# Kernel tuning notes

Hardware: AMD Instinct MI355X
Metric: run time of the kernel (lower is better)

Reference implementation:

```python
import jax, jax.numpy as jnp
import numpy as np

# ---- config (matches init_kwargs) ----
B, CIN, IMG = 4, 3, 129
PATCH, STRIDE, PAD = 4, 1, 1
DIM = CIN * PATCH * PATCH          # 48, Token_performer input dim
EMB = 256                          # out_channel -> in_dim -> emb
M = EMB // 2                       # kernel_ratio=0.5 random features
UP = 2                             # up_scale
EPS = 1e-8


def layernorm(x, g, b):
    mu = x.mean(-1, keepdims=True)
    var = ((x - mu) ** 2).mean(-1, keepdims=True)
    return (x - mu) / jnp.sqrt(var + 1e-5) * g + b


def unfold(x, k=PATCH, pad=PAD):
    # torch nn.Unfold, stride=1: output [B, C*k*k, L*L], channel order (c, kh, kw)
    Bs, C, H, W = x.shape
    xp = jnp.pad(x, ((0, 0), (0, 0), (pad, pad), (pad, pad)))
    L = H + 2 * pad - k + 1
    cols = jnp.stack([xp[:, :, i:i + L, j:j + L]
                      for i in range(k) for j in range(k)], axis=2)  # [B,C,k*k,L,L]
    return cols.reshape(Bs, C * k * k, L * L)


def prm_exp(x, w):
    # Performer positive random features: exp(w@x - |x|^2/2)/sqrt(m)
    xd = 0.5 * jnp.sum(x * x, axis=-1, keepdims=True)          # [B,T,1]
    wtx = jnp.einsum('btd,md->btm', x, w)                       # [B,T,M]
    return jnp.exp(wtx - xd) / jnp.sqrt(jnp.float32(w.shape[0]))


def upsample_bilinear_ac(x, scale):
    # nn.UpsamplingBilinear2d => align_corners=True
    Bs, C, H, W = x.shape
    Ho, Wo = H * scale, W * scale
    def coords(n_in, n_out):
        f = jnp.arange(n_out, dtype=jnp.float32) * (n_in - 1) / (n_out - 1)
        i0 = jnp.clip(jnp.floor(f).astype(jnp.int32), 0, n_in - 2)
        return i0, f - i0.astype(jnp.float32)
    h0, th = coords(H, Ho)
    w0, tw = coords(W, Wo)
    xh = x[:, :, h0, :] * (1 - th)[None, None, :, None] + x[:, :, h0 + 1, :] * th[None, None, :, None]
    return xh[:, :, :, w0] * (1 - tw) + xh[:, :, :, w0 + 1] * tw


def setup_inputs() -> dict:
    key = jax.random.key(0)
    ks = jax.random.split(key, 8)
    def n(k, shape, s=0.02):
        return jax.random.normal(k, shape, dtype=jnp.float32) * s
    return dict(
        x=jax.random.normal(ks[0], (B, CIN, IMG, IMG), dtype=jnp.float32),
        g1=jnp.ones((DIM,), jnp.float32), b1=jnp.zeros((DIM,), jnp.float32),
        w_kqv=n(ks[1], (DIM, 3 * EMB)), b_kqv=jnp.zeros((3 * EMB,), jnp.float32),
        w_prm=jax.random.normal(ks[2], (M, EMB), dtype=jnp.float32) * 0.7,  # ~ orthogonal*sqrt(m)
        w_proj=n(ks[3], (EMB, EMB)), b_proj=jnp.zeros((EMB,), jnp.float32),
        g2=jnp.ones((EMB,), jnp.float32), b2=jnp.zeros((EMB,), jnp.float32),
        w_mlp1=n(ks[4], (EMB, EMB)), b_mlp1=jnp.zeros((EMB,), jnp.float32),
        w_mlp2=n(ks[5], (EMB, EMB)), b_mlp2=jnp.zeros((EMB,), jnp.float32),
    )


def reference(x, g1, b1, w_kqv, b_kqv, w_prm, w_proj, b_proj, g2, b2,
              w_mlp1, b_mlp1, w_mlp2, b_mlp2):
    Bs = x.shape[0]
    t = unfold(x).transpose(0, 2, 1)                     # [B, T, DIM], T = 128*128
    h = layernorm(t, g1, b1)
    kqv = h @ w_kqv + b_kqv                              # [B, T, 3*EMB]
    k, q, v = jnp.split(kqv, 3, axis=-1)                 # torch split order: k, q, v
    kp, qp = prm_exp(k, w_prm), prm_exp(q, w_prm)        # [B, T, M]
    D = jnp.einsum('btm,bm->bt', qp, kp.sum(axis=1))[..., None]   # [B,T,1]
    kptv = jnp.einsum('btn,btm->bnm', v, kp)             # [B, EMB, M]
    y = jnp.einsum('btm,bnm->btn', qp, kptv) / (D + EPS) # [B, T, EMB]
    y = v + (y @ w_proj + b_proj)                        # skip uses v
    z = layernorm(y, g2, b2)
    y = y + (jax.nn.gelu(z @ w_mlp1 + b_mlp1, approximate=False) @ w_mlp2 + b_mlp2)
    T = y.shape[1]
    S = int(np.sqrt(T))
    img = y.transpose(0, 2, 1).reshape(Bs, EMB, S, S)    # [B, 256, 128, 128]
    return upsample_bilinear_ac(img, UP)                 # [B, 256, 256, 256]
```

## Files before the change

kernel.cpp:

```cpp
#include <hip/hip_runtime.h>
#include <math.h>

#define TOK   16384
#define DIM   48
#define EMB   256
#define MF    128
#define IMGsz 129

typedef __attribute__((ext_vector_type(8))) short    bf16x8;
typedef __attribute__((ext_vector_type(8))) unsigned short u16x8;
typedef __attribute__((ext_vector_type(4))) float    f32x4;

__device__ __forceinline__ ushort f2bf(float f) {
    union { float f; unsigned u; } v; v.f = f;
    unsigned u = v.u;
    return (ushort)((u + 0x7fffu + ((u >> 16) & 1u)) >> 16);
}
__device__ __forceinline__ float bf2f(ushort h) {
    union { unsigned u; float f; } v; v.u = ((unsigned)h) << 16; return v.f;
}

#define SWZ64(r,c)  ((r)*64  + (((((c)>>3) ^ ((r)&7)) & 7) << 3) + ((c)&7))
#define SWZ256(r,c) ((r)*256 + (((((c)>>3) ^ ((r)&7))) << 3) + ((c)&7))

__device__ __forceinline__ int fragmajor(int n, int k, int KC) {
    return (((n >> 4)*KC + (k >> 5))*4 + ((k >> 3) & 3))*128 + (n & 15)*8 + (k & 7);
}

__global__ __launch_bounds__(256) void kprep(
    const float* __restrict__ w_kqv, const float* __restrict__ b_kqv,
    const float* __restrict__ w_prm,
    const float* __restrict__ w_mlp1, const float* __restrict__ w_mlp2,
    ushort* __restrict__ Wbig, ushort* __restrict__ wT2, float* __restrict__ bkq)
{
    __shared__ float redp[64][4];
    int blk = blockIdx.x, tid = threadIdx.x;
    if (blk < 256) {
        if (tid < 64) {
            float v = (tid < DIM) ? w_kqv[tid*768 + 512 + blk] : 0.f;
            Wbig[fragmajor(blk, tid, 2)] = f2bf(v);
        }
    } else if (blk < 512) {
        int isQ = (blk >= 384);
        int m = blk - (isQ ? 384 : 256);
        int d = tid & 63, part = tid >> 6;
        float s = 0.f;
        if (d < 48) {
            const float* wr = w_kqv + d*768 + (isQ ? 256 : 0);
            const float* pr = w_prm + m*256;
            for (int n = part*64; n < part*64 + 64; n++) s += wr[n]*pr[n];
        }
        redp[d][part] = s;
        __syncthreads();
        if (tid < 64)
            Wbig[fragmajor((isQ ? 384 : 256) + m, tid, 2)] =
                f2bf(redp[tid][0]+redp[tid][1]+redp[tid][2]+redp[tid][3]);
    } else if (blk < 640) {
        int isQ = (blk >= 576);
        int j = blk - (isQ ? 576 : 512);
        int i = tid & 63, part = tid >> 6;
        int off = isQ ? 256 : 0;
        float s = 0.f;
        for (int n = part*64; n < part*64 + 64; n++) {
            float wi = (i < 48) ? w_kqv[i*768 + off + n] : (i == 48 ? b_kqv[off + n] : 0.f);
            float wj = (j < 48) ? w_kqv[j*768 + off + n] : (j == 48 ? b_kqv[off + n] : 0.f);
            s += wi*wj;
        }
        redp[i][part] = s;
        __syncthreads();
        if (tid < 64)
            Wbig[fragmajor((isQ ? 576 : 512) + j, tid, 2)] =
                f2bf(redp[tid][0]+redp[tid][1]+redp[tid][2]+redp[tid][3]);
    } else if (blk < 1152) {
        int w = (blk >= 896);
        int n = blk - (w ? 896 : 640);
        const float* src = w ? w_mlp2 : w_mlp1;
        wT2[w*65536 + fragmajor(n, tid, 8)] = f2bf(src[tid*256 + n]);
    } else {
        float s = 0.f;
        int m = tid & 127, off = (tid >= 128) ? 256 : 0;
        for (int n = 0; n < 256; n++) s += w_prm[m*256 + n]*b_kqv[off + n];
        bkq[tid] = s;
    }
}

__global__ __launch_bounds__(256, 3) void k1_mfma(
    const float* __restrict__ x, const float* __restrict__ g1, const float* __restrict__ b1,
    const ushort* __restrict__ Wbig, const float* __restrict__ b_kqv,
    const float* __restrict__ bkq,
    ushort* __restrict__ vfrag_out, ushort* __restrict__ vT_out,
    ushort* __restrict__ kpT_out, ushort* __restrict__ qp_out)
{
    __shared__ __align__(16) ushort h_bf[32*64];
    __shared__ __align__(16) ushort vt_bf[32*256];
    __shared__ float xdp[4][32][2];
    __shared__ float xd2[32][2];
    __shared__ float red1[32][8], red2[32][8];
    __shared__ float mu_s[32], iv_s[32];
    float* t_s = (float*)vt_bf;

    const int blk = blockIdx.x;
    const int b  = blk >> 9;
    const int t0 = (blk & 511) << 5;
    const int tid = threadIdx.x;
    const int wid = tid >> 6;
    const int l15 = tid & 15, l4 = (tid >> 4) & 3;

    for (int e = tid; e < 32*DIM; e += 256) {
        int tok = e / DIM, j = e - tok*DIM;
        int t = t0 + tok;
        int lh = t >> 7, lw = t & 127;
        int c = j >> 4, kh = (j >> 2) & 3, kw = j & 3;
        int ih = lh + kh - 1, iw = lw + kw - 1;
        float val = 0.f;
        if (ih >= 0 && ih < IMGsz && iw >= 0 && iw < IMGsz)
            val = x[((b*3 + c)*IMGsz + ih)*IMGsz + iw];
        t_s[tok*DIM + j] = val;
    }
    __syncthreads();

    {
        int tg = tid >> 3, sl = tid & 7;
        const float* tr = &t_s[tg*DIM + sl*6];
        float s1 = 0.f, s2 = 0.f;
        #pragma unroll
        for (int j = 0; j < 6; j++) { float a = tr[j]; s1 += a; s2 = fmaf(a, a, s2); }
        red1[tg][sl] = s1; red2[tg][sl] = s2;
        __syncthreads();
        if (tid < 32) {
            float a = 0.f, q = 0.f;
            #pragma unroll
            for (int j = 0; j < 8; j++) { a += red1[tid][j]; q += red2[tid][j]; }
            float mu = a * (1.f/DIM);
            mu_s[tid] = mu;
            iv_s[tid] = rsqrtf(q*(1.f/DIM) - mu*mu + 1e-5f);
        }
        __syncthreads();
        float mu = mu_s[tg], iv = iv_s[tg];
        float hv[6];
        #pragma unroll
        for (int j = 0; j < 6; j++) hv[j] = (tr[j]-mu)*iv;
        #pragma unroll
        for (int j = 0; j < 6; j++) {
            int c = sl*6 + j;
            h_bf[SWZ64(tg, c)] = f2bf(hv[j]*g1[c] + b1[c]);
        }
        int c0 = 48 + sl*2;
        h_bf[SWZ64(tg, c0    )] = (sl == 0) ? (ushort)0x3F80 : (ushort)0;
        h_bf[SWZ64(tg, c0 + 1)] = 0;
    }
    __syncthreads();

    f32x4 acc[10][2];
    #pragma unroll
    for (int j = 0; j < 10; j++)
        #pragma unroll
        for (int m = 0; m < 2; m++) { acc[j][m][0]=0.f; acc[j][m][1]=0.f; acc[j][m][2]=0.f; acc[j][m][3]=0.f; }
    #pragma unroll
    for (int kc = 0; kc < 2; kc++) {
        int ch = ((kc*4 + l4) ^ (l15 & 7)) << 3;
        bf16x8 a0 = *(const bf16x8*)&h_bf[ l15      *64 + ch];
        bf16x8 a1 = *(const bf16x8*)&h_bf[(16 + l15)*64 + ch];
        #pragma unroll
        for (int j = 0; j < 10; j++) {
            int tile = wid + 4*j;
            bf16x8 bb = *(const bf16x8*)&Wbig[(((tile*2 + kc)*4 + l4)*16 + l15)*8];
            acc[j][0] = __builtin_amdgcn_mfma_f32_16x16x32_bf16(a0, bb, acc[j][0], 0, 0, 0);
            acc[j][1] = __builtin_amdgcn_mfma_f32_16x16x32_bf16(a1, bb, acc[j][1], 0, 0, 0);
        }
    }

    #pragma unroll
    for (int j = 0; j < 4; j++) {
        int col = (wid + 4*j)*16 + l15;
        float bias = b_kqv[512 + col];
        #pragma unroll
        for (int m = 0; m < 2; m++)
            #pragma unroll
            for (int r = 0; r < 4; r++) {
                int row = m*16 + l4*4 + r;
                vt_bf[row*256 + col] = f2bf(acc[j][m][r] + bias);
            }
    }
    #pragma unroll
    for (int m = 0; m < 2; m++)
        #pragma unroll
        for (int r = 0; r < 4; r++) {
            int row = m*16 + l4*4 + r;
            float hv = bf2f(h_bf[SWZ64(row, wid*16 + l15)]);
            float sk = acc[8][m][r]*hv, sq = acc[9][m][r]*hv;
            #pragma unroll
            for (int msk = 8; msk >= 1; msk >>= 1) {
                sk += __shfl_xor(sk, msk);
                sq += __shfl_xor(sq, msk);
            }
            if (l15 == 0) { xdp[wid][row][0] = sk; xdp[wid][row][1] = sq; }
        }
    __syncthreads();
    if (tid < 64) {
        int row = tid >> 1, ty = tid & 1;
        xd2[row][ty] = 0.5f*(xdp[0][row][ty] + xdp[1][row][ty] + xdp[2][row][ty] + xdp[3][row][ty]);
    }

    {
        ushort* dst = vT_out + ((size_t)(b*EMB + tid))*TOK + t0;
        #pragma unroll
        for (int t8 = 0; t8 < 4; t8++) {
            u16x8 pk8;
            #pragma unroll
            for (int j = 0; j < 8; j++) pk8[j] = vt_bf[(t8*8 + j)*256 + tid];
            *(u16x8*)&dst[t8*8] = pk8;
        }
    }
    {
        u16x8 pk8[4];
        #pragma unroll
        for (int m = 0; m < 2; m++)
            #pragma unroll
            for (int nt = 0; nt < 4; nt++)
                #pragma unroll
                for (int r = 0; r < 4; r++) {
                    int row = m*16 + l4*4 + r;
                    int col = wid*64 + nt*16 + l15;
                    int idx = m*16 + nt*4 + r;
                    pk8[idx >> 3][idx & 7] = vt_bf[row*256 + col];
                }
        ushort* dst = vfrag_out + (size_t)blk*8192 + tid*32;
        #pragma unroll
        for (int i = 0; i < 4; i++) *(u16x8*)&dst[i*8] = pk8[i];
    }
    __syncthreads();

    const float scale = 0.08838834764831845f;
    #pragma unroll
    for (int j = 4; j < 6; j++) {
        int mcol = (wid + 4*j)*16 + l15 - 256;
        float bias = bkq[mcol];
        #pragma unroll
        for (int m = 0; m < 2; m++)
            #pragma unroll
            for (int r = 0; r < 4; r++) {
                int row = m*16 + l4*4 + r;
                vt_bf[row*256 + mcol] = f2bf(expf(acc[j][m][r] + bias - xd2[row][0]) * scale);
            }
    }
    #pragma unroll
    for (int j = 6; j < 8; j++) {
        int mcol = (wid + 4*j)*16 + l15 - 384;
        float bias = bkq[128 + mcol];
        #pragma unroll
        for (int m = 0; m < 2; m++)
            #pragma unroll
            for (int r = 0; r < 4; r++) {
                int row = m*16 + l4*4 + r;
                qp_out[(size_t)(b*TOK + t0 + row)*MF + mcol] =
                    f2bf(expf(acc[j][m][r] + bias - xd2[row][1]) * scale);
            }
    }
    __syncthreads();

    if (tid < 128) {
        ushort* dst = kpT_out + ((size_t)(b*MF + tid))*TOK + t0;
        #pragma unroll
        for (int t8 = 0; t8 < 4; t8++) {
            u16x8 pk8;
            #pragma unroll
            for (int j = 0; j < 8; j++) pk8[j] = vt_bf[(t8*8 + j)*256 + tid];
            *(u16x8*)&dst[t8*8] = pk8;
        }
    }
}

__global__ __launch_bounds__(256) void k2_ksum(const ushort* __restrict__ kpT, float* __restrict__ ksum)
{
    __shared__ float red[4];
    int blk = blockIdx.x;
    int b = blk >> 7, m = blk & 127;
    int tid = threadIdx.x;
    const ushort* row = kpT + (size_t)(b*MF + m)*TOK;
    float s = 0.f;
    for (int i = tid; i < TOK/8; i += 256) {
        u16x8 v = *(const u16x8*)&row[i*8];
        #pragma unroll
        for (int j = 0; j < 8; j++) s += bf2f(v[j]);
    }
    #pragma unroll
    for (int msk = 32; msk >= 1; msk >>= 1) s += __shfl_xor(s, msk);
    if ((tid & 63) == 0) red[tid >> 6] = s;
    __syncthreads();
    if (tid == 0) ksum[b*MF + m] = red[0] + red[1] + red[2] + red[3];
}

__global__ __launch_bounds__(256) void k3_kptv_mfma(
    const ushort* __restrict__ vT, const ushort* __restrict__ kpT, float* __restrict__ part)
{
    int blk = blockIdx.x;
    int b = blk >> 6, ns = (blk >> 5) & 1, kc = blk & 31;
    const int tid = threadIdx.x;
    const int wid = tid >> 6;
    const int l15 = tid & 15, l4 = (tid >> 4) & 3;
    const int t0 = kc * 512;
    const int n0 = ns*128 + wid*32;

    f32x4 acc[2][8];
    #pragma unroll
    for (int m = 0; m < 2; m++)
        #pragma unroll
        for (int n = 0; n < 8; n++) { acc[m][n][0]=0.f; acc[m][n][1]=0.f; acc[m][n][2]=0.f; acc[m][n][3]=0.f; }

    #pragma unroll
    for (int ks = 0; ks < 16; ks++) {
        int k0 = t0 + ks*32 + l4*8;
        bf16x8 a0 = *(const bf16x8*)&vT[((size_t)(b*EMB + n0      + l15))*TOK + k0];
        bf16x8 a1 = *(const bf16x8*)&vT[((size_t)(b*EMB + n0 + 16 + l15))*TOK + k0];
        #pragma unroll
        for (int nt = 0; nt < 8; nt++) {
            bf16x8 bb = *(const bf16x8*)&kpT[((size_t)(b*MF + nt*16 + l15))*TOK + k0];
            acc[0][nt] = __builtin_amdgcn_mfma_f32_16x16x32_bf16(a0, bb, acc[0][nt], 0, 0, 0);
            acc[1][nt] = __builtin_amdgcn_mfma_f32_16x16x32_bf16(a1, bb, acc[1][nt], 0, 0, 0);
        }
    }
    #pragma unroll
    for (int mt = 0; mt < 2; mt++)
        #pragma unroll
        for (int nt = 0; nt < 8; nt++) {
            int n = n0 + mt*16 + l4*4;
            int m = nt*16 + l15;
            #pragma unroll
            for (int r = 0; r < 4; r++)
                part[(size_t)kc*131072 + (size_t)((b*EMB + n + r)*MF + m)] = acc[mt][nt][r];
        }
}

__global__ __launch_bounds__(256) void k3r_reduce(const float* __restrict__ part, float* __restrict__ kptv)
{
    int e = blockIdx.x*256 + threadIdx.x;
    float s = 0.f;
    #pragma unroll 8
    for (int kc = 0; kc < 32; kc++) s += part[(size_t)kc*131072 + e];
    kptv[e] = s;
}

__global__ __launch_bounds__(256) void k3c_combine(
    const float* __restrict__ kptv, const float* __restrict__ w_proj, ushort* __restrict__ C_bf)
{
    __shared__ float kp_s[256][8];
    int blk = blockIdx.x;
    int b = blk >> 4, m0 = (blk & 15)*8;
    int tid = threadIdx.x;

    #pragma unroll
    for (int pass = 0; pass < 8; pass++) {
        int n1 = pass*32 + (tid >> 3);
        kp_s[n1][tid & 7] = kptv[b*32768 + n1*128 + m0 + (tid & 7)];
    }
    __syncthreads();

    float acc[8];
    #pragma unroll
    for (int j = 0; j < 8; j++) acc[j] = 0.f;
    for (int n1 = 0; n1 < 256; n1++) {
        float w = w_proj[n1*256 + tid];
        #pragma unroll
        for (int j = 0; j < 8; j++) acc[j] = fmaf(kp_s[n1][j], w, acc[j]);
    }
    u16x8 pk;
    #pragma unroll
    for (int j = 0; j < 8; j++) pk[j] = f2bf(acc[j]);
    int base = (((tid >> 4)*4 + (m0 >> 5))*4 + ((m0 >> 3) & 3))*128 + (tid & 15)*8;
    *(u16x8*)&C_bf[b*32768 + base] = pk;
}

template<int K>
__device__ __forceinline__ void gemm32(const ushort* A_s, const ushort* __restrict__ B,
                                       f32x4 acc[2][4], int l15, int l4, int wid)
{
    __builtin_amdgcn_s_setprio(1);
    #pragma unroll
    for (int kc = 0; kc < (K >> 5); kc++) {
        const int ch = ((kc*4 + l4) ^ (l15 & 7)) << 3;
        bf16x8 a0 = *(const bf16x8*)&A_s[ l15      *256 + ch];
        bf16x8 a1 = *(const bf16x8*)&A_s[(16 + l15)*256 + ch];
        #pragma unroll
        for (int nt = 0; nt < 4; nt++) {
            int ntile = wid*4 + nt;
            bf16x8 bb = *(const bf16x8*)&B[(((ntile*(K >> 5) + kc)*4 + l4)*16 + l15)*8];
            acc[0][nt] = __builtin_amdgcn_mfma_f32_16x16x32_bf16(a0, bb, acc[0][nt], 0, 0, 0);
            acc[1][nt] = __builtin_amdgcn_mfma_f32_16x16x32_bf16(a1, bb, acc[1][nt], 0, 0, 0);
        }
    }
    __builtin_amdgcn_s_setprio(0);
}

__global__ __launch_bounds__(256, 4) void k4_attn_tail(
    const ushort* __restrict__ qp, const ushort* __restrict__ vfrag,
    const float* __restrict__ ksum, const ushort* __restrict__ C_bf,
    const ushort* __restrict__ wT2,
    const float* __restrict__ b_proj,
    const float* __restrict__ g2, const float* __restrict__ b2,
    const float* __restrict__ b_mlp1, const float* __restrict__ b_mlp2,
    float* __restrict__ img2)
{
    __shared__ __align__(16) ushort A_s[16448];
    __shared__ float D_s[32];
    __shared__ float redD[32][8];
    __shared__ float red1[4][32], red2[4][32];
    __shared__ float mu_s[32], iv_s[32];

    const int blk = blockIdx.x;
    const int b  = blk >> 9;
    const int t0 = (blk & 511) << 5;
    const int tid = threadIdx.x;
    const int wid = tid >> 6;
    const int lane = tid & 63;
    const int l15 = lane & 15, l4 = lane >> 4;

    u16x8 vreg[4];
    {
        const ushort* vf = vfrag + (size_t)blk*8192 + tid*32;
        #pragma unroll
        for (int i = 0; i < 4; i++) vreg[i] = *(const u16x8*)&vf[i*8];
    }
    float bp[4];
    #pragma unroll
    for (int nt = 0; nt < 4; nt++) bp[nt] = b_proj[wid*64 + nt*16 + l15];

    {
        int tk = tid >> 3, seg = tid & 7;
        const ushort* qrow = qp + (size_t)(b*TOK + t0 + tk)*MF + seg*16;
        u16x8 q0 = *(const u16x8*)&qrow[0];
        u16x8 q1 = *(const u16x8*)&qrow[8];
        const float* ks = ksum + b*MF + seg*16;
        float dd = 0.f;
        #pragma unroll
        for (int j = 0; j < 8; j++) {
            dd = fmaf(bf2f(q0[j]), ks[j],   dd);
            dd = fmaf(bf2f(q1[j]), ks[j+8], dd);
        }
        redD[tk][seg] = dd;
        int xr = tk & 7;
        *(u16x8*)&A_s[tk*256 + (((seg*2  ) ^ xr) << 3)] = q0;
        *(u16x8*)&A_s[tk*256 + (((seg*2+1) ^ xr) << 3)] = q1;
    }
    __syncthreads();
    if (tid < 32) {
        float s = 0.f;
        #pragma unroll
        for (int j = 0; j < 8; j++) s += redD[tid][j];
        D_s[tid] = s + 1e-8f;
    }

    f32x4 acc[2][4];
    #define ZACC() { _Pragma("unroll") for (int m_=0;m_<2;m_++) _Pragma("unroll") for (int n_=0;n_<4;n_++) { acc[m_][n_][0]=0.f;acc[m_][n_][1]=0.f;acc[m_][n_][2]=0.f;acc[m_][n_][3]=0.f; } }

    ZACC();
    gemm32<MF>(A_s, C_bf + (size_t)b*32768, acc, l15, l4, wid);
    __syncthreads();
    float y2[2][4][4];
    #pragma unroll
    for (int nt = 0; nt < 4; nt++) {
        #pragma unroll
        for (int m = 0; m < 2; m++)
            #pragma unroll
            for (int r = 0; r < 4; r++) {
                int row = m*16 + l4*4 + r;
                int idx = m*16 + nt*4 + r;
                y2[m][nt][r] = acc[m][nt][r]/D_s[row] + bp[nt] + bf2f(vreg[idx >> 3][idx & 7]);
            }
    }

    {
        #pragma unroll
        for (int m = 0; m < 2; m++)
            #pragma unroll
            for (int r = 0; r < 4; r++) {
                float s1 = 0.f, s2 = 0.f;
                #pragma unroll
                for (int nt = 0; nt < 4; nt++) {
                    float a = y2[m][nt][r];
                    s1 += a; s2 = fmaf(a, a, s2);
                }
                #pragma unroll
                for (int msk = 8; msk >= 1; msk >>= 1) {
                    s1 += __shfl_xor(s1, msk);
                    s2 += __shfl_xor(s2, msk);
                }
                if (l15 == 0) {
                    int row = m*16 + l4*4 + r;
                    red1[wid][row] = s1; red2[wid][row] = s2;
                }
            }
        __syncthreads();
        if (tid < 32) {
            float a = red1[0][tid] + red1[1][tid] + red1[2][tid] + red1[3][tid];
            float q = red2[0][tid] + red2[1][tid] + red2[2][tid] + red2[3][tid];
            float mu = a * (1.f/EMB);
            mu_s[tid] = mu;
            iv_s[tid] = rsqrtf(q*(1.f/EMB) - mu*mu + 1e-5f);
        }
        __syncthreads();
        #pragma unroll
        for (int nt = 0; nt < 4; nt++) {
            int col = wid*64 + nt*16 + l15;
            float gg = g2[col], bb = b2[col];
            #pragma unroll
            for (int m = 0; m < 2; m++)
                #pragma unroll
                for (int r = 0; r < 4; r++) {
                    int row = m*16 + l4*4 + r;
                    A_s[SWZ256(row, col)] = f2bf((y2[m][nt][r] - mu_s[row])*iv_s[row]*gg + bb);
                }
        }
    }
    __syncthreads();

    ZACC();
    gemm32<EMB>(A_s, wT2, acc, l15, l4, wid);
    __syncthreads();
    #pragma unroll
    for (int nt = 0; nt < 4; nt++) {
        int col = wid*64 + nt*16 + l15;
        float bm = b_mlp1[col];
        #pragma unroll
        for (int m = 0; m < 2; m++)
            #pragma unroll
            for (int r = 0; r < 4; r++) {
                int row = m*16 + l4*4 + r;
                float a = acc[m][nt][r] + bm;
                A_s[SWZ256(row, col)] = f2bf(0.5f*a*(1.f + erff(a*0.70710678118654752f)));
            }
    }
    __syncthreads();

    ZACC();
    gemm32<EMB>(A_s, wT2 + 65536, acc, l15, l4, wid);
    #pragma unroll
    for (int nt = 0; nt < 4; nt++) {
        int col = wid*64 + nt*16 + l15;
        float bm = b_mlp2[col];
        #pragma unroll
        for (int m = 0; m < 2; m++)
            #pragma unroll
            for (int r = 0; r < 4; r++)
                y2[m][nt][r] += acc[m][nt][r] + bm;
    }
    __syncthreads();

    float* A_f = (float*)A_s;
    #pragma unroll
    for (int nt = 0; nt < 4; nt++) {
        int col = wid*64 + nt*16 + l15;
        #pragma unroll
        for (int m = 0; m < 2; m++)
            #pragma unroll
            for (int r = 0; r < 4; r++)
                A_f[(m*16 + l4*4 + r)*257 + col] = y2[m][nt][r];
    }
    __syncthreads();
    {
        int tq = tid & 7, cb = tid >> 3;
        #pragma unroll
        for (int pass = 0; pass < 8; pass++) {
            int c = pass*32 + cb;
            f32x4 pk;
            #pragma unroll
            for (int j = 0; j < 4; j++) pk[j] = A_f[(tq*4 + j)*257 + c];
            *(f32x4*)&img2[((size_t)(b*EMB + c))*TOK + t0 + tq*4] = pk;
        }
    }
}

__global__ __launch_bounds__(256) void k6_upsample(const float* __restrict__ img2, float* __restrict__ out)
{
    int idx = blockIdx.x*256 + threadIdx.x;
    int wq = idx & 63;
    int ho = (idx >> 6) & 255;
    int c  = (idx >> 14) & 255;
    int b  = idx >> 22;
    const float sc = 127.f/255.f;
    float fh = ho * sc; int h0 = (int)fh; if (h0 > 126) h0 = 126; float th = fh - h0;
    int wo = wq*4;
    int w0[4]; float tw[4];
    #pragma unroll
    for (int j = 0; j < 4; j++) {
        float fw = (wo + j) * sc;
        int w = (int)fw; if (w > 126) w = 126;
        w0[j] = w; tw[j] = fw - w;
    }
    int wsrt = w0[0] > 124 ? 124 : w0[0];
    const float* p = img2 + (((size_t)(b*EMB + c))*128 + h0)*128 + wsrt;
    f32x4 r0 = *(const f32x4*)p;
    f32x4 r1 = *(const f32x4*)(p + 128);
    f32x4 o;
    #pragma unroll
    for (int j = 0; j < 4; j++) {
        int i = w0[j] - wsrt;
        float a00 = (i == 0) ? r0[0] : ((i == 1) ? r0[1] : r0[2]);
        float a01 = (i == 0) ? r0[1] : ((i == 1) ? r0[2] : r0[3]);
        float a10 = (i == 0) ? r1[0] : ((i == 1) ? r1[1] : r1[2]);
        float a11 = (i == 0) ? r1[1] : ((i == 1) ? r1[2] : r1[3]);
        float top = fmaf(a01 - a00, tw[j], a00);
        float bot = fmaf(a11 - a10, tw[j], a10);
        o[j] = fmaf(bot - top, th, top);
    }
    *(f32x4*)&out[(size_t)idx*4] = o;
}

extern "C" void kernel_launch(void* const* d_in, const int* in_sizes, int n_in,
                              void* d_out, int out_size, void* d_ws, size_t ws_size,
                              hipStream_t stream)
{
    const float* x      = (const float*)d_in[0];
    const float* g1     = (const float*)d_in[1];
    const float* b1     = (const float*)d_in[2];
    const float* w_kqv  = (const float*)d_in[3];
    const float* b_kqv  = (const float*)d_in[4];
    const float* w_prm  = (const float*)d_in[5];
    const float* w_proj = (const float*)d_in[6];
    const float* b_proj = (const float*)d_in[7];
    const float* g2     = (const float*)d_in[8];
    const float* b2     = (const float*)d_in[9];
    const float* w_mlp1 = (const float*)d_in[10];
    const float* b_mlp1 = (const float*)d_in[11];
    const float* w_mlp2 = (const float*)d_in[12];
    const float* b_mlp2 = (const float*)d_in[13];
    float* out = (float*)d_out;
    float* ws  = (float*)d_ws;

    ushort* vfrag    = (ushort*)(ws);
    ushort* qp_bf    = (ushort*)(ws + 8388608);
    ushort* vT_bf    = (ushort*)(ws + 12582912);
    ushort* kpT_bf   = (ushort*)(ws + 20971520);
    float*  img2     = ws + 12582912;
    float*  ksum     = ws + 29360128;
    ushort* Wbig     = (ushort*)(ws + 29360640);
    ushort* wT2      = (ushort*)(ws + 29381120);
    float*  bkq      = ws + 29446656;
    float*  kptv_f32 = ws + 29446912;
    ushort* C_bf     = (ushort*)(ws + 29577984);
    float*  part     = ws + 29610752;

    hipLaunchKernelGGL(kprep, dim3(1153), dim3(256), 0, stream,
                       w_kqv, b_kqv, w_prm, w_mlp1, w_mlp2, Wbig, wT2, bkq);
    hipLaunchKernelGGL(k1_mfma, dim3(2048), dim3(256), 0, stream,
                       x, g1, b1, Wbig, b_kqv, bkq, vfrag, vT_bf, kpT_bf, qp_bf);
    hipLaunchKernelGGL(k2_ksum, dim3(512), dim3(256), 0, stream, kpT_bf, ksum);
    hipLaunchKernelGGL(k3_kptv_mfma, dim3(256), dim3(256), 0, stream, vT_bf, kpT_bf, part);
    hipLaunchKernelGGL(k3r_reduce, dim3(512), dim3(256), 0, stream, part, kptv_f32);
    hipLaunchKernelGGL(k3c_combine, dim3(64), dim3(256), 0, stream, kptv_f32, w_proj, C_bf);
    hipLaunchKernelGGL(k4_attn_tail, dim3(2048), dim3(256), 0, stream,
                       qp_bf, vfrag, ksum, C_bf, wT2, b_proj, g2, b2,
                       b_mlp1, b_mlp2, img2);
    hipLaunchKernelGGL(k6_upsample, dim3(65536), dim3(256), 0, stream, img2, out);
}
```

Before: 277.8 us.

## Drop duplicate V copy and store intermediate image in bf16

k1 now writes V only once, in a per-block channel-major layout that both k3 (kptv GEMM) and k4 (residual add) read, instead of writing a transposed vT copy plus a fragment-major copy. The k4 output image fed to the upsample kernel is stored as bf16 instead of fp32, halving that intermediate's write and read traffic. The cost is an extra bf16 rounding on the pre-upsample activations, plus narrower 4-element loads in k4 and scalar bf16 loads in upsample.

```diff
diff --git a/kernel.cpp b/kernel.cpp
--- a/kernel.cpp
+++ b/kernel.cpp
@@ -9,6 +9,7 @@
 
 typedef __attribute__((ext_vector_type(8))) short    bf16x8;
 typedef __attribute__((ext_vector_type(8))) unsigned short u16x8;
+typedef __attribute__((ext_vector_type(4))) unsigned short u16x4;
 typedef __attribute__((ext_vector_type(4))) float    f32x4;
 
 __device__ __forceinline__ ushort f2bf(float f) {
@@ -88,8 +89,7 @@
     const float* __restrict__ x, const float* __restrict__ g1, const float* __restrict__ b1,
     const ushort* __restrict__ Wbig, const float* __restrict__ b_kqv,
     const float* __restrict__ bkq,
-    ushort* __restrict__ vfrag_out, ushort* __restrict__ vT_out,
-    ushort* __restrict__ kpT_out, ushort* __restrict__ qp_out)
+    ushort* __restrict__ vfrag_out, ushort* __restrict__ kpT_out, ushort* __restrict__ qp_out)
 {
     __shared__ __align__(16) ushort h_bf[32*64];
     __shared__ __align__(16) ushort vt_bf[32*256];
@@ -203,7 +203,7 @@
     }
 
     {
-        ushort* dst = vT_out + ((size_t)(b*EMB + tid))*TOK + t0;
+        ushort* dst = vfrag_out + (size_t)blk*8192 + tid*32;
         #pragma unroll
         for (int t8 = 0; t8 < 4; t8++) {
             u16x8 pk8;
@@ -211,23 +211,6 @@
             for (int j = 0; j < 8; j++) pk8[j] = vt_bf[(t8*8 + j)*256 + tid];
             *(u16x8*)&dst[t8*8] = pk8;
         }
-    }
-    {
-        u16x8 pk8[4];
-        #pragma unroll
-        for (int m = 0; m < 2; m++)
-            #pragma unroll
-            for (int nt = 0; nt < 4; nt++)
-                #pragma unroll
-                for (int r = 0; r < 4; r++) {
-                    int row = m*16 + l4*4 + r;
-                    int col = wid*64 + nt*16 + l15;
-                    int idx = m*16 + nt*4 + r;
-                    pk8[idx >> 3][idx & 7] = vt_bf[row*256 + col];
-                }
-        ushort* dst = vfrag_out + (size_t)blk*8192 + tid*32;
-        #pragma unroll
-        for (int i = 0; i < 4; i++) *(u16x8*)&dst[i*8] = pk8[i];
     }
     __syncthreads();
 
@@ -292,7 +275,7 @@
 }
 
 __global__ __launch_bounds__(256) void k3_kptv_mfma(
-    const ushort* __restrict__ vT, const ushort* __restrict__ kpT, float* __restrict__ part)
+    const ushort* __restrict__ vfrag, const ushort* __restrict__ kpT, float* __restrict__ part)
 {
     int blk = blockIdx.x;
     int b = blk >> 6, ns = (blk >> 5) & 1, kc = blk & 31;
@@ -311,8 +294,9 @@
     #pragma unroll
     for (int ks = 0; ks < 16; ks++) {
         int k0 = t0 + ks*32 + l4*8;
-        bf16x8 a0 = *(const bf16x8*)&vT[((size_t)(b*EMB + n0      + l15))*TOK + k0];
-        bf16x8 a1 = *(const bf16x8*)&vT[((size_t)(b*EMB + n0 + 16 + l15))*TOK + k0];
+        const ushort* vt = vfrag + (size_t)(b*512 + kc*16 + ks)*8192 + l4*8;
+        bf16x8 a0 = *(const bf16x8*)&vt[(n0      + l15)*32];
+        bf16x8 a1 = *(const bf16x8*)&vt[(n0 + 16 + l15)*32];
         #pragma unroll
         for (int nt = 0; nt < 8; nt++) {
             bf16x8 bb = *(const bf16x8*)&kpT[((size_t)(b*MF + nt*16 + l15))*TOK + k0];
@@ -399,7 +383,7 @@
     const float* __restrict__ b_proj,
     const float* __restrict__ g2, const float* __restrict__ b2,
     const float* __restrict__ b_mlp1, const float* __restrict__ b_mlp2,
-    float* __restrict__ img2)
+    ushort* __restrict__ img2b)
 {
     __shared__ __align__(16) ushort A_s[16448];
     __shared__ float D_s[32];
@@ -415,11 +399,14 @@
     const int lane = tid & 63;
     const int l15 = lane & 15, l4 = lane >> 4;
 
-    u16x8 vreg[4];
+    u16x4 vreg[8];
     {
-        const ushort* vf = vfrag + (size_t)blk*8192 + tid*32;
-        #pragma unroll
-        for (int i = 0; i < 4; i++) vreg[i] = *(const u16x8*)&vf[i*8];
+        const ushort* vf = vfrag + (size_t)blk*8192 + l4*4;
+        #pragma unroll
+        for (int nt = 0; nt < 4; nt++)
+            #pragma unroll
+            for (int m = 0; m < 2; m++)
+                vreg[nt*2 + m] = *(const u16x4*)&vf[(wid*64 + nt*16 + l15)*32 + m*16];
     }
     float bp[4];
     #pragma unroll
@@ -464,8 +451,7 @@
             #pragma unroll
             for (int r = 0; r < 4; r++) {
                 int row = m*16 + l4*4 + r;
-                int idx = m*16 + nt*4 + r;
-                y2[m][nt][r] = acc[m][nt][r]/D_s[row] + bp[nt] + bf2f(vreg[idx >> 3][idx & 7]);
+                y2[m][nt][r] = acc[m][nt][r]/D_s[row] + bp[nt] + bf2f(vreg[nt*2 + m][r]);
             }
     }
 
@@ -562,15 +548,15 @@
         #pragma unroll
         for (int pass = 0; pass < 8; pass++) {
             int c = pass*32 + cb;
-            f32x4 pk;
-            #pragma unroll
-            for (int j = 0; j < 4; j++) pk[j] = A_f[(tq*4 + j)*257 + c];
-            *(f32x4*)&img2[((size_t)(b*EMB + c))*TOK + t0 + tq*4] = pk;
-        }
-    }
-}
-
-__global__ __launch_bounds__(256) void k6_upsample(const float* __restrict__ img2, float* __restrict__ out)
+            u16x4 pk;
+            #pragma unroll
+            for (int j = 0; j < 4; j++) pk[j] = f2bf(A_f[(tq*4 + j)*257 + c]);
+            *(u16x4*)&img2b[((size_t)(b*EMB + c))*TOK + t0 + tq*4] = pk;
+        }
+    }
+}
+
+__global__ __launch_bounds__(256) void k6_upsample(const ushort* __restrict__ img2b, float* __restrict__ out)
 {
     int idx = blockIdx.x*256 + threadIdx.x;
     int wq = idx & 63;
@@ -588,9 +574,10 @@
         w0[j] = w; tw[j] = fw - w;
     }
     int wsrt = w0[0] > 124 ? 124 : w0[0];
-    const float* p = img2 + (((size_t)(b*EMB + c))*128 + h0)*128 + wsrt;
-    f32x4 r0 = *(const f32x4*)p;
-    f32x4 r1 = *(const f32x4*)(p + 128);
+    const ushort* p = img2b + (((size_t)(b*EMB + c))*128 + h0)*128 + wsrt;
+    float r0[4], r1[4];
+    #pragma unroll
+    for (int j = 0; j < 4; j++) { r0[j] = bf2f(p[j]); r1[j] = bf2f(p[128 + j]); }
     f32x4 o;
     #pragma unroll
     for (int j = 0; j < 4; j++) {
@@ -629,27 +616,26 @@
 
     ushort* vfrag    = (ushort*)(ws);
     ushort* qp_bf    = (ushort*)(ws + 8388608);
-    ushort* vT_bf    = (ushort*)(ws + 12582912);
-    ushort* kpT_bf   = (ushort*)(ws + 20971520);
-    float*  img2     = ws + 12582912;
-    float*  ksum     = ws + 29360128;
-    ushort* Wbig     = (ushort*)(ws + 29360640);
-    ushort* wT2      = (ushort*)(ws + 29381120);
-    float*  bkq      = ws + 29446656;
-    float*  kptv_f32 = ws + 29446912;
-    ushort* C_bf     = (ushort*)(ws + 29577984);
-    float*  part     = ws + 29610752;
+    ushort* kpT_bf   = (ushort*)(ws + 12582912);
+    ushort* img2b    = (ushort*)(ws + 16777216);
+    float*  ksum     = ws + 25165824;
+    ushort* Wbig     = (ushort*)(ws + 25166336);
+    ushort* wT2      = (ushort*)(ws + 25186816);
+    float*  bkq      = ws + 25252352;
+    float*  kptv_f32 = ws + 25252608;
+    ushort* C_bf     = (ushort*)(ws + 25383680);
+    float*  part     = ws + 25416448;
 
     hipLaunchKernelGGL(kprep, dim3(1153), dim3(256), 0, stream,
                        w_kqv, b_kqv, w_prm, w_mlp1, w_mlp2, Wbig, wT2, bkq);
     hipLaunchKernelGGL(k1_mfma, dim3(2048), dim3(256), 0, stream,
-                       x, g1, b1, Wbig, b_kqv, bkq, vfrag, vT_bf, kpT_bf, qp_bf);
+                       x, g1, b1, Wbig, b_kqv, bkq, vfrag, kpT_bf, qp_bf);
     hipLaunchKernelGGL(k2_ksum, dim3(512), dim3(256), 0, stream, kpT_bf, ksum);
-    hipLaunchKernelGGL(k3_kptv_mfma, dim3(256), dim3(256), 0, stream, vT_bf, kpT_bf, part);
+    hipLaunchKernelGGL(k3_kptv_mfma, dim3(256), dim3(256), 0, stream, vfrag, kpT_bf, part);
     hipLaunchKernelGGL(k3r_reduce, dim3(512), dim3(256), 0, stream, part, kptv_f32);
     hipLaunchKernelGGL(k3c_combine, dim3(64), dim3(256), 0, stream, kptv_f32, w_proj, C_bf);
     hipLaunchKernelGGL(k4_attn_tail, dim3(2048), dim3(256), 0, stream,
                        qp_bf, vfrag, ksum, C_bf, wT2, b_proj, g2, b2,
-                       b_mlp1, b_mlp2, img2);
-    hipLaunchKernelGGL(k6_upsample, dim3(65536), dim3(256), 0, stream, img2, out);
-}
+                       b_mlp1, b_mlp2, img2b);
+    hipLaunchKernelGGL(k6_upsample, dim3(65536), dim3(256), 0, stream, img2b, out);
+}
```

Result: faster. 261.9 us (median of 2 runs) (-5.7%).
